# Kernel tuning notes

Measured on AMD Instinct MI355X. Metric: run time of the kernel, lower is better.

Reference implementation:

```python
import jax, jax.numpy as jnp
import numpy as np

N_NODES = 50000
N_EDGES = 1600000
GL = [512, 256, 16]
LL = [16, 16]


def setup_inputs() -> dict:
    key = jax.random.key(0)
    ks = jax.random.split(key, 10)
    H = jax.random.normal(ks[0], (N_NODES, GL[0]), dtype=jnp.float32)
    edge_index = jax.random.randint(ks[1], (2, N_EDGES), 0, N_NODES, dtype=jnp.int64)
    edge_vals = jax.random.uniform(ks[2], (N_EDGES,), dtype=jnp.float32)
    def uni(k, shape, fan_out):
        stdv = 1.0 / np.sqrt(fan_out)
        return jax.random.uniform(k, shape, minval=-stdv, maxval=stdv, dtype=jnp.float32)
    W1 = uni(ks[3], (GL[0], GL[1]), GL[1])
    b1 = uni(ks[4], (GL[1],), GL[1])
    W2 = uni(ks[5], (GL[1], GL[2]), GL[2])
    b2 = uni(ks[6], (GL[2],), GL[2])
    Wl = uni(ks[7], (LL[0], LL[1]), LL[0])
    bl = uni(ks[8], (LL[1],), LL[0])
    return {"H": H, "edge_index": edge_index, "edge_vals": edge_vals,
            "W1": W1, "b1": b1, "W2": W2, "b2": b2, "Wl": Wl, "bl": bl}


def reference(H, edge_index, edge_vals, W1, b1, W2, b2, Wl, bl):
    row, col = edge_index[0], edge_index[1]
    n = H.shape[0]

    def spmm(X):  # (A @ X) for sparse COO A, X: [N, d]
        return jax.ops.segment_sum(edge_vals[:, None] * X[col], row, num_segments=n)

    # graph conv layers (dropout condition idx < len-2 never fires with 2 layers)
    H1 = jax.nn.relu(spmm(H @ W1) + b1)
    H2 = jax.nn.relu(spmm(H1 @ W2) + b2)
    # linear head
    H3 = jax.nn.relu(H2 @ Wl + bl)
    Y = jax.nn.softmax(H3, axis=1)  # [N, g]

    # NCut loss: sum_e w_e * dot(Y[row_e]/Gamma, (1-Y)[col_e])
    D = jax.ops.segment_sum(edge_vals, row, num_segments=n)  # degree [N]
    Gamma = Y.T @ D  # [g]
    YbyG = Y / Gamma[None, :]
    loss = jnp.sum(jnp.sum(YbyG[row] * (1.0 - Y)[col], axis=1) * edge_vals)
    return jnp.reshape(loss, (1,))
```

## Files before the change

kernel.cpp:

```cpp
#include <hip/hip_runtime.h>


constexpr int NN = 50000;
constexpr int NE = 1600000;
constexpr int F0 = 512;
constexpr int F1 = 256;
constexpr int G  = 16;
constexpr int CB   = 196;
constexpr int CCAP = 10240;
constexpr int CHUNK = 4096;
constexpr int NPASS = 391;

typedef short  s16x8 __attribute__((ext_vector_type(8)));
typedef float  f32x4 __attribute__((ext_vector_type(4)));
typedef float  f32x2 __attribute__((ext_vector_type(2)));
typedef int    i32x4 __attribute__((ext_vector_type(4)));
typedef int    i32x2 __attribute__((ext_vector_type(2)));
typedef float  fv4   __attribute__((ext_vector_type(4)));

static __device__ __forceinline__ unsigned short f2bf(float f) {
    union { float f; unsigned u; } v; v.f = f;
    unsigned r = (v.u + 0x7FFFu + ((v.u >> 16) & 1u)) >> 16;
    return (unsigned short)r;
}
static __device__ __forceinline__ float bf2f(unsigned short u) {
    union { unsigned u; float f; } v; v.u = (unsigned)u << 16;
    return v.f;
}

static __device__ __forceinline__ void glds16(const void* g, void* l) {
    __builtin_amdgcn_global_load_lds(
        (const __attribute__((address_space(1))) unsigned int*)g,
        (__attribute__((address_space(3))) unsigned int*)l,
        16, 0, 0);
}

static __device__ __forceinline__ s16x8 pack8(f32x4 a, f32x4 b) {
    union { unsigned u[4]; s16x8 v; } r;
    asm("v_cvt_pk_bf16_f32 %0, %1, %2" : "=v"(r.u[0]) : "v"(a.x), "v"(a.y));
    asm("v_cvt_pk_bf16_f32 %0, %1, %2" : "=v"(r.u[1]) : "v"(a.z), "v"(a.w));
    asm("v_cvt_pk_bf16_f32 %0, %1, %2" : "=v"(r.u[2]) : "v"(b.x), "v"(b.y));
    asm("v_cvt_pk_bf16_f32 %0, %1, %2" : "=v"(r.u[3]) : "v"(b.z), "v"(b.w));
    return r.v;
}

__global__ __launch_bounds__(256) void k_castW1(const float* __restrict__ W1, unsigned short* __restrict__ W1t) {
    int idx = blockIdx.x * 256 + threadIdx.x;
    if (idx < F0 * F1) {
        int k = idx >> 8, n = idx & 255;
        W1t[n * F0 + k] = f2bf(W1[idx]);
    }
}

__global__ __launch_bounds__(256) void k_fused1(const float* __restrict__ H,
                                                const unsigned short* __restrict__ W1t,
                                                unsigned char* __restrict__ XW,
                                                const int* __restrict__ row, const int* __restrict__ col,
                                                const float* __restrict__ ev,
                                                int* __restrict__ ccur, int2* __restrict__ cbuf) {
    __shared__ __align__(16) unsigned char smem[49152];
    const int bid = blockIdx.x;
    const int tid = threadIdx.x;
    const int stripe = bid / 3;
    const int pos = bid - stripe * 3;

    if (pos != 1) {
        const int gidx = stripe * 2 + (pos >> 1);
        const int lane = tid & 63;
        const int wave = tid >> 6;
        const int bm = (gidx >> 1) * 128;
        const int bn = (gidx & 1) * 128;
        const int m_off = (wave & 1) * 64;
        const int n_off = (wave >> 1) * 64;
        const int l15  = lane & 15;
        const int quad = lane >> 4;

        f32x4 acc[4][4];
#pragma unroll
        for (int i = 0; i < 4; ++i)
#pragma unroll
            for (int j = 0; j < 4; ++j) acc[i][j] = (f32x4)0.f;

        const int arow16 = tid >> 4;
        const int slA    = (tid & 15) ^ (arow16 & 7);
        const int browB  = tid >> 3;
        const int slB    = (tid & 7) ^ (browB & 7);
        const int wvB    = wave * 1024;

#define STAGE(K0)                                                              \
        do {                                                                   \
            _Pragma("unroll")                                                  \
            for (int p = 0; p < 8; ++p) {                                      \
                int gr = bm + p * 16 + arow16;                                 \
                gr = gr < NN ? gr : NN - 1;                                    \
                glds16(&H[(size_t)gr * F0 + (K0) + slA * 4],                   \
                       smem + p * 4096 + wvB);                                 \
            }                                                                  \
            _Pragma("unroll")                                                  \
            for (int p = 0; p < 4; ++p)                                        \
                glds16(&W1t[(size_t)(bn + p * 32 + browB) * F0 + (K0) + slB * 8], \
                       smem + 32768 + p * 4096 + wvB);                         \
        } while (0)

        STAGE(0);
        asm volatile("s_waitcnt vmcnt(0)" ::: "memory");
        __syncthreads();
        for (int k0 = 0; k0 < F0; k0 += 64) {
#pragma unroll
            for (int kk6 = 0; kk6 < 2; ++kk6) {
                const int kk = kk6 * 32;
                s16x8 af[4], bfr[4];
#pragma unroll
                for (int mi = 0; mi < 4; ++mi) {
                    const int r = m_off + mi * 16 + l15;
                    const int sw = r & 7;
                    const int s0 = (kk >> 2) + quad * 2;
                    const char* rb = (const char*)smem + r * 256;
                    f32x4 v0 = *(const f32x4*)(rb + (((s0    ) ^ sw) << 4));
                    f32x4 v1 = *(const f32x4*)(rb + (((s0 + 1) ^ sw) << 4));
                    af[mi] = pack8(v0, v1);
                }
#pragma unroll
                for (int ni = 0; ni < 4; ++ni) {
                    const int r = n_off + ni * 16 + l15;
                    const int sb = (kk >> 3) + quad;
                    bfr[ni] = *(const s16x8*)((const char*)smem + 32768 + r * 128
                                              + ((sb ^ (r & 7)) << 4));
                }
#pragma unroll
                for (int mi = 0; mi < 4; ++mi)
#pragma unroll
                    for (int ni = 0; ni < 4; ++ni)
                        acc[mi][ni] = __builtin_amdgcn_mfma_f32_16x16x32_bf16(af[mi], bfr[ni], acc[mi][ni], 0, 0, 0);
            }
            __syncthreads();
            if (k0 + 64 < F0) {
                STAGE(k0 + 64);
                asm volatile("s_waitcnt vmcnt(0)" ::: "memory");
            }
            __syncthreads();
        }
#undef STAGE
#pragma unroll
        for (int mi = 0; mi < 4; ++mi) {
            int r0 = bm + m_off + mi * 16 + quad * 4;
#pragma unroll
            for (int reg = 0; reg < 4; ++reg) {
                int gr = r0 + reg;
                if (gr < NN) {
                    unsigned char* orow = &XW[(size_t)gr * F1 + bn + n_off];
#pragma unroll
                    for (int ni = 0; ni < 4; ++ni) {
                        int pk = __builtin_amdgcn_cvt_pk_fp8_f32(acc[mi][ni][reg], 0.f, 0, false);
                        orow[ni * 16 + l15] = (unsigned char)(pk & 0xff);
                    }
                }
            }
        }
    } else {
        int* hcnt  = (int*)smem;
        int* hbase = hcnt + CB;
        for (int i = tid; i < CB; i += 256) hcnt[i] = 0;
        __syncthreads();

        const int base4 = stripe * (CHUNK / 4);
        int recx[16]; float recw[16]; int cb[16];
#pragma unroll
        for (int k = 0; k < 4; ++k) {
            int i4 = base4 + k * 256 + tid;
            bool ok = i4 < NE / 4;
            i32x4 r = ok ? __builtin_nontemporal_load(&((const i32x4*)row)[i4]) : (i32x4)0;
            i32x4 c = ok ? __builtin_nontemporal_load(&((const i32x4*)col)[i4]) : (i32x4)0;
            fv4   w = ok ? __builtin_nontemporal_load(&((const fv4*)ev)[i4])   : (fv4)0.f;
            int rr[4] = {r.x, r.y, r.z, r.w};
            int cc[4] = {c.x, c.y, c.z, c.w};
            float ww[4] = {w.x, w.y, w.z, w.w};
#pragma unroll
            for (int j = 0; j < 4; ++j) {
                int slot = k * 4 + j;
                if (ok) {
                    cb[slot] = rr[j] >> 8;
                    atomicAdd(&hcnt[cb[slot]], 1);
                } else {
                    cb[slot] = -1;
                }
                recx[slot] = (cc[j] << 16) | (rr[j] & 255);
                recw[slot] = ww[j];
            }
        }
        __syncthreads();
        for (int i = tid; i < CB; i += 256) {
            int cnt = hcnt[i];
            hbase[i] = (cnt > 0) ? atomicAdd(&ccur[i], cnt) : 0;
            hcnt[i] = 0;
        }
        __syncthreads();
#pragma unroll
        for (int slot = 0; slot < 16; ++slot) {
            if (cb[slot] >= 0) {
                int p = hbase[cb[slot]] + atomicAdd(&hcnt[cb[slot]], 1);
                cbuf[(size_t)cb[slot] * CCAP + p] = make_int2(recx[slot], __float_as_int(recw[slot]));
            }
        }
    }
}

__global__ __launch_bounds__(256) void k_passB(const int2* __restrict__ cbuf, const int* __restrict__ ccur,
                                               int* __restrict__ rowptr, int2* __restrict__ E) {
    __shared__ int cnt[256];
    __shared__ int scn[256];
    __shared__ int red[4];
    const int cbk = blockIdx.x;
    const int tid = threadIdx.x;
    cnt[tid] = 0;

    int b = 0;
    for (int i = tid; i < cbk; i += 256) b += ccur[i];
#pragma unroll
    for (int off = 1; off < 64; off <<= 1) b += __shfl_xor(b, off, 64);
    if ((tid & 63) == 0) red[tid >> 6] = b;
    __syncthreads();
    const int base = red[0] + red[1] + red[2] + red[3];

    const int total = ccur[cbk];
    const int2* src = cbuf + (size_t)cbk * CCAP;
    for (int i = tid; i < total; i += 256) atomicAdd(&cnt[src[i].x & 255], 1);
    __syncthreads();

    scn[tid] = cnt[tid];
    __syncthreads();
    for (int off = 1; off < 256; off <<= 1) {
        int t = (tid >= off) ? scn[tid - off] : 0;
        __syncthreads();
        scn[tid] += t;
        __syncthreads();
    }
    const int excl = scn[tid] - cnt[tid];
    const int r = (cbk << 8) + tid;
    if (r <= NN) rowptr[r] = base + excl;
    __syncthreads();
    cnt[tid] = base + excl;
    __syncthreads();
    for (int i = tid; i < total; i += 256) {
        int2 rec = src[i];
        int rl = rec.x & 255;
        int c  = (int)((unsigned)rec.x >> 16);
        int p = atomicAdd(&cnt[rl], 1);
        E[p] = make_int2(c << 8, rec.y);
    }
}

__global__ __launch_bounds__(256) void k_spmm1(const unsigned char* __restrict__ XW, const int* __restrict__ rowptr,
                                               const int2* __restrict__ E,
                                               const float* __restrict__ b1, const float* __restrict__ W2,
                                               unsigned short* __restrict__ Z, float* __restrict__ Dv) {
    __shared__ float W2T[G * F1];
    const int tid = threadIdx.x;
#pragma unroll
    for (int it = 0; it < 16; ++it)
        W2T[it * 256 + tid] = W2[tid * 16 + it];
    __syncthreads();
    const int lane16 = tid & 15;
    const int loff = lane16 * 16;
    const int n = blockIdx.x * 16 + (tid >> 4);
    const int s = rowptr[n];
    const int e = rowptr[n + 1];
    const i32x2* Ev = (const i32x2*)E;

    float acc[16];
#pragma unroll
    for (int q = 0; q < 16; ++q) acc[q] = 0.f;
    float wsum = 0.f;

    for (int i = s; i < e; i += 4) {
        int of[4]; float w[4];
#pragma unroll
        for (int k = 0; k < 4; ++k) {
            int idx = i + k;
            bool ok = idx < e;
            i32x2 ed = __builtin_nontemporal_load(&Ev[ok ? idx : s]);
            of[k] = ed.x; w[k] = ok ? __int_as_float(ed.y) : 0.f;
        }
        uint4 gg[4];
#pragma unroll
        for (int k = 0; k < 4; ++k)
            gg[k] = *(const uint4*)(XW + of[k] + loff);
#pragma unroll
        for (int k = 0; k < 4; ++k) {
            const unsigned gw[4] = {gg[k].x, gg[k].y, gg[k].z, gg[k].w};
#pragma unroll
            for (int q = 0; q < 4; ++q) {
                f32x2 lo = __builtin_amdgcn_cvt_pk_f32_fp8(gw[q], false);
                f32x2 hi = __builtin_amdgcn_cvt_pk_f32_fp8(gw[q], true);
                acc[q * 4 + 0] = fmaf(w[k], lo.x, acc[q * 4 + 0]);
                acc[q * 4 + 1] = fmaf(w[k], lo.y, acc[q * 4 + 1]);
                acc[q * 4 + 2] = fmaf(w[k], hi.x, acc[q * 4 + 2]);
                acc[q * 4 + 3] = fmaf(w[k], hi.y, acc[q * 4 + 3]);
            }
            wsum += w[k];
        }
    }
    if (lane16 == 0) Dv[n] = wsum;

#pragma unroll
    for (int q = 0; q < 4; ++q) {
        float4 bb = *(const float4*)&b1[loff + q * 4];
        acc[q * 4 + 0] = fmaxf(acc[q * 4 + 0] + bb.x, 0.f);
        acc[q * 4 + 1] = fmaxf(acc[q * 4 + 1] + bb.y, 0.f);
        acc[q * 4 + 2] = fmaxf(acc[q * 4 + 2] + bb.z, 0.f);
        acc[q * 4 + 3] = fmaxf(acc[q * 4 + 3] + bb.w, 0.f);
    }

    float p[G];
#pragma unroll
    for (int j = 0; j < G; ++j) {
        float pj = 0.f;
#pragma unroll
        for (int q = 0; q < 4; ++q) {
            float4 w4 = *(const float4*)&W2T[j * F1 + loff + q * 4];
            pj += acc[q * 4 + 0] * w4.x + acc[q * 4 + 1] * w4.y
                + acc[q * 4 + 2] * w4.z + acc[q * 4 + 3] * w4.w;
        }
        p[j] = pj;
    }
#pragma unroll
    for (int off = 1; off < 16; off <<= 1) {
#pragma unroll
        for (int j = 0; j < G; ++j) p[j] += __shfl_xor(p[j], off, 64);
    }
    if (lane16 == 0) {
        unsigned zp[8];
#pragma unroll
        for (int j = 0; j < 8; ++j)
            zp[j] = (unsigned)f2bf(p[2 * j]) | ((unsigned)f2bf(p[2 * j + 1]) << 16);
        uint4* zo = (uint4*)&Z[n * G];
        zo[0] = make_uint4(zp[0], zp[1], zp[2], zp[3]);
        zo[1] = make_uint4(zp[4], zp[5], zp[6], zp[7]);
    }
}

__global__ __launch_bounds__(256) void k_head(const unsigned short* __restrict__ Zb, const int* __restrict__ rowptr,
                                              const int2* __restrict__ E,
                                              const float* __restrict__ b2, const float* __restrict__ Wl,
                                              const float* __restrict__ bl, const float* __restrict__ Dv,
                                              unsigned short* __restrict__ Yb, float* __restrict__ GammaP) {
    __shared__ float WlS[G * G];
    __shared__ float gsh[G];
    const int tid = threadIdx.x;
    if (tid < G * G) WlS[tid] = Wl[tid];
    if (tid < G) gsh[tid] = 0.f;
    __syncthreads();
    const int lane = tid & 63;
    const int g = lane >> 3;
    const int d = lane & 7;
    const int n = blockIdx.x * 4 + (tid >> 6);
    const int s = __builtin_amdgcn_readfirstlane(rowptr[n]);
    const int e = __builtin_amdgcn_readfirstlane(rowptr[n + 1]);
    const char* Zc = (const char*)Zb;
    const i32x2* Ev = (const i32x2*)E;

    float a0 = 0.f, a1 = 0.f;
    for (int base = s; base < e; base += 16) {
        int i0 = base + g;
        int i1 = base + 8 + g;
        i32x2 e0 = __builtin_nontemporal_load(&Ev[(i0 < e) ? i0 : s]);
        i32x2 e1 = __builtin_nontemporal_load(&Ev[(i1 < e) ? i1 : s]);
        float w0 = (i0 < e) ? __int_as_float(e0.y) : 0.f;
        float w1 = (i1 < e) ? __int_as_float(e1.y) : 0.f;
        unsigned z0 = *(const unsigned*)(Zc + (e0.x >> 3) + d * 4);
        unsigned z1 = *(const unsigned*)(Zc + (e1.x >> 3) + d * 4);
        a0 = fmaf(w0, bf2f((unsigned short)(z0 & 0xffff)), a0);
        a1 = fmaf(w0, bf2f((unsigned short)(z0 >> 16)), a1);
        a0 = fmaf(w1, bf2f((unsigned short)(z1 & 0xffff)), a0);
        a1 = fmaf(w1, bf2f((unsigned short)(z1 >> 16)), a1);
    }
    a0 += __shfl_xor(a0, 8, 64);  a1 += __shfl_xor(a1, 8, 64);
    a0 += __shfl_xor(a0, 16, 64); a1 += __shfl_xor(a1, 16, 64);
    a0 += __shfl_xor(a0, 32, 64); a1 += __shfl_xor(a1, 32, 64);

    const int j = lane & 15;
    float e0v = __shfl(a0, j >> 1, 64);
    float e1v = __shfl(a1, j >> 1, 64);
    float accj = (j & 1) ? e1v : e0v;

    float h2 = fmaxf(accj + b2[j], 0.f);
    float s3 = 0.f;
#pragma unroll
    for (int k = 0; k < G; ++k) s3 = fmaf(__shfl(h2, k, 64), WlS[k * G + j], s3);
    float h3 = fmaxf(s3 + bl[j], 0.f);
    float m = h3;
    m = fmaxf(m, __shfl_xor(m, 1, 64));
    m = fmaxf(m, __shfl_xor(m, 2, 64));
    m = fmaxf(m, __shfl_xor(m, 4, 64));
    m = fmaxf(m, __shfl_xor(m, 8, 64));
    float ex = __expf(h3 - m);
    float se = ex;
    se += __shfl_xor(se, 1, 64);
    se += __shfl_xor(se, 2, 64);
    se += __shfl_xor(se, 4, 64);
    se += __shfl_xor(se, 8, 64);
    float y = ex / se;
    if (lane < G) {
        Yb[n * G + j] = f2bf(y);
        atomicAdd(&gsh[j], y * Dv[n]);
    }
    __syncthreads();
    if (tid < G) atomicAdd(&GammaP[(blockIdx.x & 63) * G + tid], gsh[tid]);
}

__global__ __launch_bounds__(256) void k_loss(const unsigned short* __restrict__ Yb, const int* __restrict__ rowptr,
                                              const int2* __restrict__ E, float* __restrict__ SjP) {
    __shared__ float sjsh[G];
    const int tid = threadIdx.x;
    if (tid < G) sjsh[tid] = 0.f;
    __syncthreads();
    const int lane = tid & 63;
    const int g = lane >> 3;
    const int d = lane & 7;
    const int n = blockIdx.x * 4 + (tid >> 6);
    const int s = __builtin_amdgcn_readfirstlane(rowptr[n]);
    const int e = __builtin_amdgcn_readfirstlane(rowptr[n + 1]);
    const char* Yc = (const char*)Yb;
    const i32x2* Ev = (const i32x2*)E;

    unsigned yr = *(const unsigned*)(Yc + ((size_t)n << 5) + d * 4);
    float y0 = bf2f((unsigned short)(yr & 0xffff));
    float y1 = bf2f((unsigned short)(yr >> 16));

    float s0 = 0.f, s1 = 0.f;
    for (int base = s; base < e; base += 16) {
        int i0 = base + g;
        int i1 = base + 8 + g;
        i32x2 e0 = __builtin_nontemporal_load(&Ev[(i0 < e) ? i0 : s]);
        i32x2 e1 = __builtin_nontemporal_load(&Ev[(i1 < e) ? i1 : s]);
        float w0 = (i0 < e) ? __int_as_float(e0.y) : 0.f;
        float w1 = (i1 < e) ? __int_as_float(e1.y) : 0.f;
        unsigned z0 = *(const unsigned*)(Yc + (e0.x >> 3) + d * 4);
        unsigned z1 = *(const unsigned*)(Yc + (e1.x >> 3) + d * 4);
        s0 = fmaf(w0 * y0, bf2f((unsigned short)(z0 & 0xffff)), s0);
        s1 = fmaf(w0 * y1, bf2f((unsigned short)(z0 >> 16)), s1);
        s0 = fmaf(w1 * y0, bf2f((unsigned short)(z1 & 0xffff)), s0);
        s1 = fmaf(w1 * y1, bf2f((unsigned short)(z1 >> 16)), s1);
    }
    s0 += __shfl_xor(s0, 8, 64);  s1 += __shfl_xor(s1, 8, 64);
    s0 += __shfl_xor(s0, 16, 64); s1 += __shfl_xor(s1, 16, 64);
    s0 += __shfl_xor(s0, 32, 64); s1 += __shfl_xor(s1, 32, 64);
    if (lane < 8) {
        atomicAdd(&sjsh[2 * lane],     s0);
        atomicAdd(&sjsh[2 * lane + 1], s1);
    }
    __syncthreads();
    if (tid < G) atomicAdd(&SjP[(blockIdx.x & 63) * G + tid], sjsh[tid]);
}

__global__ void k_final(const float* __restrict__ GammaP, const float* __restrict__ SjP,
                        float* __restrict__ out) {
    const int tid = threadIdx.x;
    const int j = tid & 15;
    float gam = 0.f, sj = 0.f;
    for (int b = 0; b < 64; ++b) {
        gam += GammaP[b * G + j];
        sj  += SjP[b * G + j];
    }
    float v = sj / gam;
    v += __shfl_xor(v, 1, 64);
    v += __shfl_xor(v, 2, 64);
    v += __shfl_xor(v, 4, 64);
    v += __shfl_xor(v, 8, 64);
    if (tid == 0) out[0] = 16.0f - v;
}

static inline size_t alignup(size_t x) { return (x + 255) & ~(size_t)255; }

extern "C" void kernel_launch(void* const* d_in, const int* in_sizes, int n_in,
                              void* d_out, int out_size, void* d_ws, size_t ws_size,
                              hipStream_t stream) {
    const float* H  = (const float*)d_in[0];
    const int*   ei = (const int*)d_in[1];
    const float* ev = (const float*)d_in[2];
    const float* W1 = (const float*)d_in[3];
    const float* b1 = (const float*)d_in[4];
    const float* W2 = (const float*)d_in[5];
    const float* b2 = (const float*)d_in[6];
    const float* Wl = (const float*)d_in[7];
    const float* bl = (const float*)d_in[8];
    const int* row = ei;
    const int* col = ei + NE;

    char* base = (char*)d_ws;
    size_t off = 0;
    unsigned char*  XW  = (unsigned char*)(base + off);  off = alignup(off + (size_t)NN * F1);
    unsigned short* W1t = (unsigned short*)(base + off); off = alignup(off + (size_t)F0 * F1 * 2);
    unsigned short* Z   = (unsigned short*)(base + off); off = alignup(off + (size_t)NN * G * 2);
    unsigned short* Yb  = (unsigned short*)(base + off); off = alignup(off + (size_t)NN * G * 2);
    float* Dv     = (float*)(base + off); off = alignup(off + (size_t)NN * 4);
    size_t zoff = off;
    int*   ccur   = (int*)(base + off);   off += (size_t)CB * 4;
    float* GammaP = (float*)(base + off); off += (size_t)64 * G * 4;
    float* SjP    = (float*)(base + off); off += (size_t)64 * G * 4;
    size_t zsize = off - zoff;
    off = alignup(off);
    int*   rowptr = (int*)(base + off);   off = alignup(off + (size_t)(NN + 1) * 4);
    int2*  cbuf   = (int2*)(base + off);  off = alignup(off + (size_t)CB * CCAP * 8);
    int2*  E      = (int2*)(base + off);  off = alignup(off + (size_t)NE * 8);

    hipMemsetAsync(base + zoff, 0, zsize, stream);

    k_castW1<<<dim3((F0 * F1 + 255) / 256), dim3(256), 0, stream>>>(W1, W1t);
    k_fused1<<<dim3(3 * NPASS), dim3(256), 0, stream>>>(
        H, W1t, XW, row, col, ev, ccur, cbuf);
    k_passB<<<dim3(CB), dim3(256), 0, stream>>>(cbuf, ccur, rowptr, E);
    k_spmm1<<<dim3(NN / 16), dim3(256), 0, stream>>>(XW, rowptr, E, b1, W2, Z, Dv);
    k_head<<<dim3(NN / 4), dim3(256), 0, stream>>>(Z, rowptr, E, b2, Wl, bl, Dv, Yb, GammaP);
    k_loss<<<dim3(NN / 4), dim3(256), 0, stream>>>(Yb, rowptr, E, SjP);
    k_final<<<dim3(1), dim3(64), 0, stream>>>(GammaP, SjP, (float*)d_out);
}
```

Measured before the change: 375.8 us.

## Stage block edge lists in LDS and software-pipeline gathers in SpMM1

The first SpMM kernel now loads each block's contiguous edge range into shared memory cooperatively, in coalesced chunks, instead of having each 16-lane group read its edges from global memory. The gather loop is double-buffered over 8 edges at a time so the next batch of FP8 row loads is in flight while the current batch is accumulated. The W2 transpose in shared memory is padded to a stride of 20 per lane to avoid bank conflicts. The cost is more registers from the two 8-deep buffers, which may lower occupancy, plus extra block-wide barriers per chunk.

```diff
diff --git a/kernel.cpp b/kernel.cpp
--- a/kernel.cpp
+++ b/kernel.cpp
@@ -10,6 +10,7 @@
 constexpr int CCAP = 10240;
 constexpr int CHUNK = 4096;
 constexpr int NPASS = 391;
+constexpr int ECH = 1024;
 
 typedef short  s16x8 __attribute__((ext_vector_type(8)));
 typedef float  f32x4 __attribute__((ext_vector_type(4)));
@@ -254,52 +255,116 @@
                                                const int2* __restrict__ E,
                                                const float* __restrict__ b1, const float* __restrict__ W2,
                                                unsigned short* __restrict__ Z, float* __restrict__ Dv) {
-    __shared__ float W2T[G * F1];
+    __shared__ float W2P[G * 320];
+    __shared__ i32x2 Esh[ECH];
     const int tid = threadIdx.x;
 #pragma unroll
-    for (int it = 0; it < 16; ++it)
-        W2T[it * 256 + tid] = W2[tid * 16 + it];
-    __syncthreads();
+    for (int it = 0; it < 16; ++it) {
+        int elem = it * 256 + tid;
+        int j = elem >> 8;
+        int l = (elem >> 4) & 15;
+        int t = elem & 15;
+        W2P[j * 320 + l * 20 + t] = W2[(l * 16 + t) * 16 + j];
+    }
     const int lane16 = tid & 15;
     const int loff = lane16 * 16;
     const int n = blockIdx.x * 16 + (tid >> 4);
+    const int nb0 = rowptr[blockIdx.x * 16];
+    const int nb1 = rowptr[blockIdx.x * 16 + 16];
     const int s = rowptr[n];
     const int e = rowptr[n + 1];
-    const i32x2* Ev = (const i32x2*)E;
+    const i32x2* E2 = (const i32x2*)E;
 
     float acc[16];
 #pragma unroll
     for (int q = 0; q < 16; ++q) acc[q] = 0.f;
     float wsum = 0.f;
 
-    for (int i = s; i < e; i += 4) {
-        int of[4]; float w[4];
-#pragma unroll
-        for (int k = 0; k < 4; ++k) {
-            int idx = i + k;
-            bool ok = idx < e;
-            i32x2 ed = __builtin_nontemporal_load(&Ev[ok ? idx : s]);
-            of[k] = ed.x; w[k] = ok ? __int_as_float(ed.y) : 0.f;
-        }
-        uint4 gg[4];
-#pragma unroll
-        for (int k = 0; k < 4; ++k)
-            gg[k] = *(const uint4*)(XW + of[k] + loff);
-#pragma unroll
-        for (int k = 0; k < 4; ++k) {
-            const unsigned gw[4] = {gg[k].x, gg[k].y, gg[k].z, gg[k].w};
-#pragma unroll
-            for (int q = 0; q < 4; ++q) {
-                f32x2 lo = __builtin_amdgcn_cvt_pk_f32_fp8(gw[q], false);
-                f32x2 hi = __builtin_amdgcn_cvt_pk_f32_fp8(gw[q], true);
-                acc[q * 4 + 0] = fmaf(w[k], lo.x, acc[q * 4 + 0]);
-                acc[q * 4 + 1] = fmaf(w[k], lo.y, acc[q * 4 + 1]);
-                acc[q * 4 + 2] = fmaf(w[k], hi.x, acc[q * 4 + 2]);
-                acc[q * 4 + 3] = fmaf(w[k], hi.y, acc[q * 4 + 3]);
-            }
-            wsum += w[k];
-        }
-    }
+#define GATH8(GG, WW, BASE)                                        \
+        _Pragma("unroll")                                          \
+        for (int k = 0; k < 8; ++k) {                              \
+            i32x2 ed = Esh[(BASE) - w0 + k];                       \
+            WW[k] = __int_as_float(ed.y);                          \
+            GG[k] = *(const uint4*)(XW + ed.x + loff);             \
+        }
+#define COMP8(GG, WW)                                              \
+        _Pragma("unroll")                                          \
+        for (int k = 0; k < 8; ++k) {                              \
+            const unsigned gw[4] = {GG[k].x, GG[k].y, GG[k].z, GG[k].w}; \
+            _Pragma("unroll")                                      \
+            for (int q = 0; q < 4; ++q) {                          \
+                f32x2 lo = __builtin_amdgcn_cvt_pk_f32_fp8(gw[q], false); \
+                f32x2 hi = __builtin_amdgcn_cvt_pk_f32_fp8(gw[q], true);  \
+                acc[q * 4 + 0] = fmaf(WW[k], lo.x, acc[q * 4 + 0]); \
+                acc[q * 4 + 1] = fmaf(WW[k], lo.y, acc[q * 4 + 1]); \
+                acc[q * 4 + 2] = fmaf(WW[k], hi.x, acc[q * 4 + 2]); \
+                acc[q * 4 + 3] = fmaf(WW[k], hi.y, acc[q * 4 + 3]); \
+            }                                                      \
+            wsum += WW[k];                                         \
+        }
+
+    for (int w0 = nb0; w0 < nb1; w0 += ECH) {
+        const int wend = (w0 + ECH < nb1) ? (w0 + ECH) : nb1;
+        __syncthreads();
+        for (int t = tid; t < wend - w0; t += 256)
+            Esh[t] = __builtin_nontemporal_load(&E2[w0 + t]);
+        __syncthreads();
+
+        const int gs = (s > w0) ? s : w0;
+        const int ge = (e < wend) ? e : wend;
+
+        uint4 ggA[8], ggB[8];
+        float wA[8], wB[8];
+        int i = gs;
+        if (i + 8 <= ge) { GATH8(ggA, wA, i) }
+        while (i + 24 <= ge) {
+            GATH8(ggB, wB, i + 8)
+            COMP8(ggA, wA)
+            GATH8(ggA, wA, i + 16)
+            COMP8(ggB, wB)
+            i += 16;
+        }
+        if (i + 16 <= ge) {
+            GATH8(ggB, wB, i + 8)
+            COMP8(ggA, wA)
+            COMP8(ggB, wB)
+            i += 16;
+        } else if (i + 8 <= ge) {
+            COMP8(ggA, wA)
+            i += 8;
+        }
+        for (; i < ge; i += 4) {
+            int of4[4]; float w4v[4];
+#pragma unroll
+            for (int k = 0; k < 4; ++k) {
+                int idx = i + k;
+                bool ok = idx < ge;
+                i32x2 ed = Esh[(ok ? idx : gs) - w0];
+                of4[k] = ed.x; w4v[k] = ok ? __int_as_float(ed.y) : 0.f;
+            }
+            uint4 gg[4];
+#pragma unroll
+            for (int k = 0; k < 4; ++k)
+                gg[k] = *(const uint4*)(XW + of4[k] + loff);
+#pragma unroll
+            for (int k = 0; k < 4; ++k) {
+                const unsigned gw[4] = {gg[k].x, gg[k].y, gg[k].z, gg[k].w};
+#pragma unroll
+                for (int q = 0; q < 4; ++q) {
+                    f32x2 lo = __builtin_amdgcn_cvt_pk_f32_fp8(gw[q], false);
+                    f32x2 hi = __builtin_amdgcn_cvt_pk_f32_fp8(gw[q], true);
+                    acc[q * 4 + 0] = fmaf(w4v[k], lo.x, acc[q * 4 + 0]);
+                    acc[q * 4 + 1] = fmaf(w4v[k], lo.y, acc[q * 4 + 1]);
+                    acc[q * 4 + 2] = fmaf(w4v[k], hi.x, acc[q * 4 + 2]);
+                    acc[q * 4 + 3] = fmaf(w4v[k], hi.y, acc[q * 4 + 3]);
+                }
+                wsum += w4v[k];
+            }
+        }
+    }
+#undef GATH8
+#undef COMP8
+
     if (lane16 == 0) Dv[n] = wsum;
 
 #pragma unroll
@@ -317,7 +382,7 @@
         float pj = 0.f;
 #pragma unroll
         for (int q = 0; q < 4; ++q) {
-            float4 w4 = *(const float4*)&W2T[j * F1 + loff + q * 4];
+            float4 w4 = *(const float4*)&W2P[j * 320 + lane16 * 20 + q * 4];
             pj += acc[q * 4 + 0] * w4.x + acc[q * 4 + 1] * w4.y
                 + acc[q * 4 + 2] * w4.z + acc[q * 4 + 3] * w4.w;
         }
```

Result: faster. 358.7 us (-4.6%).
